# Optimization experiments

Hardware: AMD Instinct MI355X
Metric: run time of the kernel (lower is better)

Reference implementation:

```python
import jax, jax.numpy as jnp
import numpy as np

H = 512
B = 64
S = 2048

def setup_inputs() -> dict:
    key = jax.random.key(0)
    ks = jax.random.split(key, 7)
    s = 1.0 / np.sqrt(H)
    return {
        "query": jax.random.normal(ks[0], (B, H), dtype=jnp.float32),
        "ref": jax.random.normal(ks[1], (B, S, H), dtype=jnp.float32),
        "Wq": jax.random.uniform(ks[2], (H, H), dtype=jnp.float32, minval=-s, maxval=s),
        "bq": jax.random.uniform(ks[3], (H,), dtype=jnp.float32, minval=-s, maxval=s),
        "Wr": jax.random.uniform(ks[4], (H, H), dtype=jnp.float32, minval=-s, maxval=s),
        "br": jax.random.uniform(ks[5], (H,), dtype=jnp.float32, minval=-s, maxval=s),
        "V": jax.random.uniform(ks[6], (H,), dtype=jnp.float32, minval=-s, maxval=s),
    }

def reference(query, ref, Wq, bq, Wr, br, V):
    # W_ref is Conv1d(H, H, kernel=1) applied to ref permuted to [B,H,S];
    # a 1x1 conv is a per-position GEMM: out[b,o,s] = sum_h Wr[o,h] * ref[b,s,h] + br[o]
    ref_t = jnp.einsum('bsh,oh->bos', ref, Wr) + br[None, :, None]  # [B,H,S]
    q = query @ Wq.T + bq                                            # [B,H]
    # logits[b,s] = V . tanh(q[b,:] + ref_t[b,:,s])
    logits = jnp.einsum('h,bhs->bs', V, jnp.tanh(q[:, :, None] + ref_t))  # [B,S]
    # use_tanh=False -> no C*tanh clipping
    return ref_t, logits
```

## Files before the change

### kernel.cpp

```cpp
#include <hip/hip_runtime.h>

constexpr int Hd = 512;
constexpr int Bd = 64;
constexpr int Sd = 2048;

constexpr int BM = 128;
constexpr int BN = 128;
constexpr int BK = 32;
constexpr int LDP = BK + 4;

typedef __bf16 bf16x8 __attribute__((ext_vector_type(8)));
typedef float  f32x4  __attribute__((ext_vector_type(4)));
typedef unsigned short u16x8 __attribute__((ext_vector_type(8)));

__device__ __forceinline__ unsigned short f2bf(float f){
  __bf16 h = (__bf16)f;
  return __builtin_bit_cast(unsigned short, h);
}

__device__ __forceinline__ float fast_tanh(float x){
  float e = __expf(2.0f * x);
  return 1.0f - 2.0f * __builtin_amdgcn_rcpf(e + 1.0f);
}

__global__ __launch_bounds__(256) void prologue_kernel(const float* __restrict__ Wr,
                                                       unsigned short* __restrict__ Wrb,
                                                       const float* __restrict__ query,
                                                       const float* __restrict__ Wq,
                                                       const float* __restrict__ bq,
                                                       float* __restrict__ qout){
  if (blockIdx.x < 128){
    int base = (blockIdx.x*256 + (int)threadIdx.x) * 8;
    f32x4 v0 = *(const f32x4*)(Wr + base);
    f32x4 v1 = *(const f32x4*)(Wr + base + 4);
    u16x8 o;
    o[0]=f2bf(v0[0]); o[1]=f2bf(v0[1]); o[2]=f2bf(v0[2]); o[3]=f2bf(v0[3]);
    o[4]=f2bf(v1[0]); o[5]=f2bf(v1[1]); o[6]=f2bf(v1[2]); o[7]=f2bf(v1[3]);
    *(u16x8*)(Wrb + base) = o;
  } else {
    int b   = blockIdx.x - 128;
    int tid = threadIdx.x;
    __shared__ float qs[Hd];
    for (int i = tid; i < Hd; i += 256) qs[i] = query[b*Hd + i];
    __syncthreads();
    for (int o = tid; o < Hd; o += 256){
      const float* w = Wq + (size_t)o*Hd;
      float s = 0.f;
      #pragma unroll 4
      for (int k = 0; k < Hd; k += 4){
        f32x4 wv = *(const f32x4*)(w + k);
        s += wv[0]*qs[k] + wv[1]*qs[k+1] + wv[2]*qs[k+2] + wv[3]*qs[k+3];
      }
      qout[b*Hd + o] = s + bq[o];
    }
  }
}

struct SReg { u16x8 a0, a1; f32x4 b[4]; };

__global__ __launch_bounds__(256, 3) void fused_kernel(const float* __restrict__ ref,
                                                       const unsigned short* __restrict__ Wrb,
                                                       const float* __restrict__ br,
                                                       const float* __restrict__ V,
                                                       const float* __restrict__ qbuf,
                                                       float* __restrict__ out,
                                                       float* __restrict__ logits){
  const int bid = blockIdx.x;
  const int wid = (bid & 7) * (gridDim.x >> 3) + (bid >> 3);
  const int mt  = wid & 3;
  const int nt  = (wid >> 2) & 15;
  const int bb  = wid >> 6;
  const int m0  = mt * BM;
  const int n0  = nt * BN;

  const int tid  = threadIdx.x;
  const int lane = tid & 63;
  const int wave = tid >> 6;
  const int wm   = wave >> 1;
  const int wn   = wave & 1;

  __shared__ unsigned short As[BM][LDP];
  __shared__ unsigned short Bs[BN][LDP];

  f32x4 acc[4][4];
  #pragma unroll
  for (int i = 0; i < 4; ++i)
    #pragma unroll
    for (int j = 0; j < 4; ++j)
      acc[i][j] = f32x4{0.f, 0.f, 0.f, 0.f};

  const int ar = tid >> 1;
  const int ak = (tid & 1) * 16;
  const int sr = tid >> 3;
  const int sk = (tid & 7) * 4;

  const unsigned short* Ag = Wrb + (size_t)(m0 + ar)*Hd + ak;
  const float*          Bg = ref + ((size_t)bb*Sd + (n0 + sr))*Hd + sk;

  const int rofs = lane & 15;
  const int koff = (lane >> 4) * 8;

  SReg S0, S1;

  auto issue = [&](SReg& S, int kt){
    S.a0 = *(const u16x8*)(Ag + kt);
    S.a1 = *(const u16x8*)(Ag + kt + 8);
    #pragma unroll
    for (int it = 0; it < 4; ++it) S.b[it] = *(const f32x4*)(Bg + (size_t)it*32*Hd + kt);
  };
  auto write_stage = [&](const SReg& S){
    *(u16x8*)(&As[ar][ak])     = S.a0;
    *(u16x8*)(&As[ar][ak + 8]) = S.a1;
    #pragma unroll
    for (int it = 0; it < 4; ++it){
      uint2 pk;
      pk.x = (unsigned)f2bf(S.b[it][0]) | ((unsigned)f2bf(S.b[it][1]) << 16);
      pk.y = (unsigned)f2bf(S.b[it][2]) | ((unsigned)f2bf(S.b[it][3]) << 16);
      *(uint2*)(&Bs[sr + it*32][sk]) = pk;
    }
  };
  auto step = [&](SReg& S, int t){
    write_stage(S);
    int kn = t + 2; kn = (kn > 15 ? 15 : kn) * BK;
    issue(S, kn);
    asm volatile("s_waitcnt lgkmcnt(0)" ::: "memory");
    __builtin_amdgcn_s_barrier();
    bf16x8 a[4], b[4];
    #pragma unroll
    for (int mi = 0; mi < 4; ++mi)
      a[mi] = *(const bf16x8*)(&As[wm*64 + mi*16 + rofs][koff]);
    #pragma unroll
    for (int ni = 0; ni < 4; ++ni)
      b[ni] = *(const bf16x8*)(&Bs[wn*64 + ni*16 + rofs][koff]);
    #pragma unroll
    for (int mi = 0; mi < 4; ++mi)
      #pragma unroll
      for (int ni = 0; ni < 4; ++ni)
        acc[mi][ni] = __builtin_amdgcn_mfma_f32_16x16x32_bf16(a[mi], b[ni], acc[mi][ni], 0, 0, 0);
    asm volatile("s_waitcnt lgkmcnt(0)" ::: "memory");
    __builtin_amdgcn_s_barrier();
  };

  issue(S0, 0);
  issue(S1, BK);
  #pragma unroll 1
  for (int t2 = 0; t2 < 8; ++t2){
    step(S0, t2*2);
    step(S1, t2*2 + 1);
  }

  const int col0 = n0 + wn*64;
  const int row0 = m0 + wm*64;
  const int cl   = lane & 15;
  const int rgrp = (lane >> 4) * 4;
  const float* qrow = qbuf + bb*Hd;
  float colsum[4] = {0.f, 0.f, 0.f, 0.f};
  float* outb = out + (size_t)bb*Hd*Sd;

  #pragma unroll
  for (int mi = 0; mi < 4; ++mi){
    #pragma unroll
    for (int j = 0; j < 4; ++j){
      int o = row0 + mi*16 + rgrp + j;
      float brv = br[o];
      float qv  = qrow[o];
      float vv  = V[o];
      float* orow = outb + (size_t)o*Sd + col0;
      #pragma unroll
      for (int ni = 0; ni < 4; ++ni){
        float c = acc[mi][ni][j] + brv;
        __builtin_nontemporal_store(c, &orow[ni*16 + cl]);
        colsum[ni] += vv * fast_tanh(qv + c);
      }
    }
  }

  #pragma unroll
  for (int ni = 0; ni < 4; ++ni){
    colsum[ni] += __shfl_xor(colsum[ni], 16);
    colsum[ni] += __shfl_xor(colsum[ni], 32);
  }
  if (lane < 16){
    float* lrow = logits + (size_t)bb*Sd + col0;
    #pragma unroll
    for (int ni = 0; ni < 4; ++ni)
      atomicAdd(lrow + ni*16 + cl, colsum[ni]);
  }
}

extern "C" void kernel_launch(void* const* d_in, const int* in_sizes, int n_in,
                              void* d_out, int out_size, void* d_ws, size_t ws_size,
                              hipStream_t stream){
  const float* query = (const float*)d_in[0];
  const float* ref   = (const float*)d_in[1];
  const float* Wq    = (const float*)d_in[2];
  const float* bq    = (const float*)d_in[3];
  const float* Wr    = (const float*)d_in[4];
  const float* br    = (const float*)d_in[5];
  const float* V     = (const float*)d_in[6];

  float* out    = (float*)d_out;
  float* logits = out + (size_t)Bd*Hd*Sd;
  float* qbuf   = (float*)d_ws;
  unsigned short* Wrb = (unsigned short*)((char*)d_ws + 128*1024);

  hipMemsetAsync(logits, 0, (size_t)Bd*Sd*sizeof(float), stream);
  prologue_kernel<<<192, 256, 0, stream>>>(Wr, Wrb, query, Wq, bq, qbuf);

  fused_kernel<<<Bd*64, 256, 0, stream>>>(ref, Wrb, br, V, qbuf, out, logits);
}
```

Baseline: 203.9 us.

## Drop LDS staging and load GEMM operands directly into registers per wave

Removes the shared-memory tiles and block barriers from the fused GEMM. Each wave now loads its own A (bf16 weights) and B (fp32 ref, converted to bf16 in registers) fragments straight from global memory, with one-stage register prefetch of B. This eliminates LDS writes and reads and the barrier syncs, but each ref row is now fetched by both wm waves and each weight row by both wn waves, so global/L2 traffic doubles. The occupancy hint of 3 blocks per CU is also dropped.

```diff
diff --git a/kernel.cpp b/kernel.cpp
--- a/kernel.cpp
+++ b/kernel.cpp
@@ -7,7 +7,6 @@
 constexpr int BM = 128;
 constexpr int BN = 128;
 constexpr int BK = 32;
-constexpr int LDP = BK + 4;
 
 typedef __bf16 bf16x8 __attribute__((ext_vector_type(8)));
 typedef float  f32x4  __attribute__((ext_vector_type(4)));
@@ -21,6 +20,13 @@
 __device__ __forceinline__ float fast_tanh(float x){
   float e = __expf(2.0f * x);
   return 1.0f - 2.0f * __builtin_amdgcn_rcpf(e + 1.0f);
+}
+
+__device__ __forceinline__ bf16x8 cvt8(f32x4 lo, f32x4 hi){
+  bf16x8 r;
+  r[0]=(__bf16)lo[0]; r[1]=(__bf16)lo[1]; r[2]=(__bf16)lo[2]; r[3]=(__bf16)lo[3];
+  r[4]=(__bf16)hi[0]; r[5]=(__bf16)hi[1]; r[6]=(__bf16)hi[2]; r[7]=(__bf16)hi[3];
+  return r;
 }
 
 __global__ __launch_bounds__(256) void prologue_kernel(const float* __restrict__ Wr,
@@ -56,15 +62,13 @@
   }
 }
 
-struct SReg { u16x8 a0, a1; f32x4 b[4]; };
-
-__global__ __launch_bounds__(256, 3) void fused_kernel(const float* __restrict__ ref,
-                                                       const unsigned short* __restrict__ Wrb,
-                                                       const float* __restrict__ br,
-                                                       const float* __restrict__ V,
-                                                       const float* __restrict__ qbuf,
-                                                       float* __restrict__ out,
-                                                       float* __restrict__ logits){
+__global__ __launch_bounds__(256) void fused_kernel(const float* __restrict__ ref,
+                                                    const unsigned short* __restrict__ Wrb,
+                                                    const float* __restrict__ br,
+                                                    const float* __restrict__ V,
+                                                    const float* __restrict__ qbuf,
+                                                    float* __restrict__ out,
+                                                    float* __restrict__ logits){
   const int bid = blockIdx.x;
   const int wid = (bid & 7) * (gridDim.x >> 3) + (bid >> 3);
   const int mt  = wid & 3;
@@ -79,8 +83,11 @@
   const int wm   = wave >> 1;
   const int wn   = wave & 1;
 
-  __shared__ unsigned short As[BM][LDP];
-  __shared__ unsigned short Bs[BN][LDP];
+  const int r16 = lane & 15;
+  const int kg8 = (lane >> 4) * 8;
+
+  const unsigned short* Abase = Wrb + (size_t)(m0 + wm*64 + r16)*Hd + kg8;
+  const float*          Bbase = ref + ((size_t)bb*Sd + (n0 + wn*64 + r16))*Hd + kg8;
 
   f32x4 acc[4][4];
   #pragma unroll
@@ -89,64 +96,40 @@
     for (int j = 0; j < 4; ++j)
       acc[i][j] = f32x4{0.f, 0.f, 0.f, 0.f};
 
-  const int ar = tid >> 1;
-  const int ak = (tid & 1) * 16;
-  const int sr = tid >> 3;
-  const int sk = (tid & 7) * 4;
+  bf16x8 Af[4];
+  f32x4  Br[2][4][2];
 
-  const unsigned short* Ag = Wrb + (size_t)(m0 + ar)*Hd + ak;
-  const float*          Bg = ref + ((size_t)bb*Sd + (n0 + sr))*Hd + sk;
-
-  const int rofs = lane & 15;
-  const int koff = (lane >> 4) * 8;
-
-  SReg S0, S1;
-
-  auto issue = [&](SReg& S, int kt){
-    S.a0 = *(const u16x8*)(Ag + kt);
-    S.a1 = *(const u16x8*)(Ag + kt + 8);
+  auto loadA = [&](int kt){
     #pragma unroll
-    for (int it = 0; it < 4; ++it) S.b[it] = *(const f32x4*)(Bg + (size_t)it*32*Hd + kt);
+    for (int mi = 0; mi < 4; ++mi)
+      Af[mi] = *(const bf16x8*)(Abase + (size_t)mi*16*Hd + kt);
   };
-  auto write_stage = [&](const SReg& S){
-    *(u16x8*)(&As[ar][ak])     = S.a0;
-    *(u16x8*)(&As[ar][ak + 8]) = S.a1;
+  auto loadB = [&](int u, int kt){
     #pragma unroll
-    for (int it = 0; it < 4; ++it){
-      uint2 pk;
-      pk.x = (unsigned)f2bf(S.b[it][0]) | ((unsigned)f2bf(S.b[it][1]) << 16);
-      pk.y = (unsigned)f2bf(S.b[it][2]) | ((unsigned)f2bf(S.b[it][3]) << 16);
-      *(uint2*)(&Bs[sr + it*32][sk]) = pk;
+    for (int ni = 0; ni < 4; ++ni){
+      Br[u][ni][0] = *(const f32x4*)(Bbase + (size_t)ni*16*Hd + kt);
+      Br[u][ni][1] = *(const f32x4*)(Bbase + (size_t)ni*16*Hd + kt + 4);
     }
   };
-  auto step = [&](SReg& S, int t){
-    write_stage(S);
-    int kn = t + 2; kn = (kn > 15 ? 15 : kn) * BK;
-    issue(S, kn);
-    asm volatile("s_waitcnt lgkmcnt(0)" ::: "memory");
-    __builtin_amdgcn_s_barrier();
-    bf16x8 a[4], b[4];
-    #pragma unroll
-    for (int mi = 0; mi < 4; ++mi)
-      a[mi] = *(const bf16x8*)(&As[wm*64 + mi*16 + rofs][koff]);
-    #pragma unroll
-    for (int ni = 0; ni < 4; ++ni)
-      b[ni] = *(const bf16x8*)(&Bs[wn*64 + ni*16 + rofs][koff]);
-    #pragma unroll
-    for (int mi = 0; mi < 4; ++mi)
-      #pragma unroll
-      for (int ni = 0; ni < 4; ++ni)
-        acc[mi][ni] = __builtin_amdgcn_mfma_f32_16x16x32_bf16(a[mi], b[ni], acc[mi][ni], 0, 0, 0);
-    asm volatile("s_waitcnt lgkmcnt(0)" ::: "memory");
-    __builtin_amdgcn_s_barrier();
-  };
 
-  issue(S0, 0);
-  issue(S1, BK);
+  loadB(0, 0);
   #pragma unroll 1
   for (int t2 = 0; t2 < 8; ++t2){
-    step(S0, t2*2);
-    step(S1, t2*2 + 1);
+    #pragma unroll
+    for (int u = 0; u < 2; ++u){
+      const int t  = t2*2 + u;
+      const int kc = t * BK;
+      const int kn = (t + 1 < 16 ? t + 1 : 15) * BK;
+      loadA(kc);
+      loadB(u ^ 1, kn);
+      #pragma unroll
+      for (int ni = 0; ni < 4; ++ni){
+        bf16x8 Bf = cvt8(Br[u][ni][0], Br[u][ni][1]);
+        #pragma unroll
+        for (int mi = 0; mi < 4; ++mi)
+          acc[mi][ni] = __builtin_amdgcn_mfma_f32_16x16x32_bf16(Af[mi], Bf, acc[mi][ni], 0, 0, 0);
+      }
+    }
   }
 
   const int col0 = n0 + wn*64;
```

Result: slower. 423.3 us (+107.6%).
